# Kernel optimization log

Measured on AMD Instinct MI355X. Metric: run time of the kernel, lower is better.

The kernel has to match this reference:

```python
import jax, jax.numpy as jnp
import numpy as np

D_MODEL = 1024
D_FFN = 4096
N_HEAD = 16
D_K = D_MODEL // N_HEAD
EPS = 1e-10


def _layernorm(x, gamma, beta):
    mean = jnp.mean(x, axis=-1, keepdims=True)
    var = jnp.mean((x - mean) ** 2, axis=-1, keepdims=True)
    return gamma * ((x - mean) / jnp.sqrt(var + EPS)) + beta


def setup_inputs() -> dict:
    key = jax.random.key(0)
    ks = jax.random.split(key, 16)
    s = 1.0 / np.sqrt(D_MODEL)
    sf = 1.0 / np.sqrt(D_FFN)
    return {
        "x": jax.random.normal(ks[0], (4, 2048, D_MODEL), jnp.float32),
        "wq": jax.random.uniform(ks[1], (D_MODEL, D_MODEL), jnp.float32, -s, s),
        "bq": jnp.zeros((D_MODEL,), jnp.float32),
        "wk": jax.random.uniform(ks[2], (D_MODEL, D_MODEL), jnp.float32, -s, s),
        "bk": jnp.zeros((D_MODEL,), jnp.float32),
        "wv": jax.random.uniform(ks[3], (D_MODEL, D_MODEL), jnp.float32, -s, s),
        "bv": jnp.zeros((D_MODEL,), jnp.float32),
        "wo": jax.random.uniform(ks[4], (D_MODEL, D_MODEL), jnp.float32, -s, s),
        "bo": jnp.zeros((D_MODEL,), jnp.float32),
        "g1": jnp.ones((D_MODEL,), jnp.float32),
        "b1": jnp.zeros((D_MODEL,), jnp.float32),
        "w1": jax.random.uniform(ks[5], (D_MODEL, D_FFN), jnp.float32, -s, s),
        "bf1": jnp.zeros((D_FFN,), jnp.float32),
        "w2": jax.random.uniform(ks[6], (D_FFN, D_MODEL), jnp.float32, -sf, sf),
        "bf2": jnp.zeros((D_MODEL,), jnp.float32),
        "g2": jnp.ones((D_MODEL,), jnp.float32),
        "b2": jnp.zeros((D_MODEL,), jnp.float32),
    }


def reference(x, wq, bq, wk, bk, wv, bv, wo, bo, g1, b1, w1, bf1, w2, bf2, g2, b2):
    B, S, _ = x.shape
    # projections -> (B, H, S, d_k)
    q = (x @ wq + bq).reshape(B, S, N_HEAD, D_K).transpose(0, 2, 1, 3)
    k = (x @ wk + bk).reshape(B, S, N_HEAD, D_K).transpose(0, 2, 1, 3)
    v = (x @ wv + bv).reshape(B, S, N_HEAD, D_K).transpose(0, 2, 1, 3)
    score = jnp.einsum("bhqd,bhkd->bhqk", q, k) / jnp.sqrt(jnp.asarray(D_K, x.dtype))
    attn = jax.nn.softmax(score, axis=-1)
    out = jnp.einsum("bhqk,bhkd->bhqd", attn, v)
    out = out.transpose(0, 2, 1, 3).reshape(B, S, D_MODEL)
    out = out @ wo + bo
    out1 = _layernorm(x + out, g1, b1)
    # FFN (dropout is identity in eval mode)
    ff = jax.nn.relu(out1 @ w1 + bf1) @ w2 + bf2
    out2 = _layernorm(out1 + ff, g2, b2)
    return (out2, attn)
```

## Files before the change

### kernel.cpp

```cpp
#include <hip/hip_runtime.h>
#include <hip/hip_bf16.h>

#define DEV __device__ __forceinline__

typedef __attribute__((ext_vector_type(4))) float f32x4;
typedef __attribute__((ext_vector_type(8))) __bf16 bf16v;
typedef __attribute__((ext_vector_type(8))) unsigned short u16x8;
typedef __attribute__((ext_vector_type(4))) unsigned short u16x4;

DEV unsigned short f2b(float x) {
    unsigned u = __builtin_bit_cast(unsigned, x);
    unsigned r = u + 0x7FFF + ((u >> 16) & 1);
    return (unsigned short)(r >> 16);
}
DEV float b2f(unsigned short u) {
    unsigned v = (unsigned)u << 16;
    return __builtin_bit_cast(float, v);
}

DEV void gl_lds16(const void* g, void* l) {
    __builtin_amdgcn_global_load_lds(
        (const __attribute__((address_space(1))) unsigned*)g,
        (__attribute__((address_space(3))) unsigned*)l,
        16, 0, 0);
}


DEV void transp_dev(const float* __restrict__ in, unsigned short* __restrict__ out,
                    int R, int C, int bx, int by, float (*t)[33]) {
    int tx = threadIdx.x & 31, ty = threadIdx.x >> 5;
    long c0 = (long)bx * 32, r0 = (long)by * 32;
#pragma unroll
    for (int i = 0; i < 4; i++)
        t[ty + i * 8][tx] = in[(r0 + ty + i * 8) * C + c0 + tx];
    __syncthreads();
#pragma unroll
    for (int i = 0; i < 4; i++)
        out[(c0 + ty + i * 8) * R + r0 + tx] = f2b(t[tx][ty + i * 8]);
}

__global__ __launch_bounds__(256) void prep_all(
    const float* __restrict__ x, const float* __restrict__ wq,
    const float* __restrict__ wk, const float* __restrict__ wv,
    const float* __restrict__ wo, const float* __restrict__ w1,
    const float* __restrict__ w2, const float* __restrict__ bq,
    const float* __restrict__ bk, const float* __restrict__ bv,
    unsigned short* __restrict__ xb, unsigned short* __restrict__ wqkvT,
    unsigned short* __restrict__ woT, unsigned short* __restrict__ w1T,
    unsigned short* __restrict__ w2T, float* __restrict__ bqkv) {
    __shared__ float t[32][33];
    int id = blockIdx.x;
    if (id < 8192) {
        long i = ((long)id * 256 + threadIdx.x) * 4;
        float4 f = *(const float4*)(x + i);
        u16x4 u;
        u[0] = f2b(f.x); u[1] = f2b(f.y); u[2] = f2b(f.z); u[3] = f2b(f.w);
        *(u16x4*)(xb + i) = u;
        return;
    }
    id -= 8192;
    if (id < 1024) { transp_dev(wq, wqkvT, 1024, 1024, id & 31, id >> 5, t); return; }
    id -= 1024;
    if (id < 1024) { transp_dev(wk, wqkvT + 1048576, 1024, 1024, id & 31, id >> 5, t); return; }
    id -= 1024;
    if (id < 1024) { transp_dev(wv, wqkvT + 2097152, 1024, 1024, id & 31, id >> 5, t); return; }
    id -= 1024;
    if (id < 1024) { transp_dev(wo, woT, 1024, 1024, id & 31, id >> 5, t); return; }
    id -= 1024;
    if (id < 4096) { transp_dev(w1, w1T, 1024, 4096, id & 127, id >> 7, t); return; }
    id -= 4096;
    if (id < 4096) { transp_dev(w2, w2T, 4096, 1024, id & 31, id >> 5, t); return; }
    id -= 4096;
    int i = id * 256 + threadIdx.x;
    float v = (i < 1024) ? bq[i] : (i < 2048) ? bk[i - 1024] : bv[i - 2048];
    bqkv[i] = v;
}

DEV float waveSum(float v) {
#pragma unroll
    for (int o = 32; o > 0; o >>= 1) v += __shfl_xor(v, o);
    return v;
}

__global__ __launch_bounds__(256) void ln_rows(const float* __restrict__ in,
                                               const float* __restrict__ g,
                                               const float* __restrict__ b,
                                               float* __restrict__ outF,
                                               unsigned short* __restrict__ outB) {
    const float* p = in + (long)blockIdx.x * 1024;
    __shared__ float red[4], red2[4];
    int t = threadIdx.x, lane = t & 63, wave = t >> 6;
    float4 v = ((const float4*)p)[t];
    float s = v.x + v.y + v.z + v.w;
    float q = v.x * v.x + v.y * v.y + v.z * v.z + v.w * v.w;
    s = waveSum(s); q = waveSum(q);
    if (lane == 0) { red[wave] = s; red2[wave] = q; }
    __syncthreads();
    s = red[0] + red[1] + red[2] + red[3];
    q = red2[0] + red2[1] + red2[2] + red2[3];
    float mean = s * (1.0f / 1024.0f);
    float var = q * (1.0f / 1024.0f) - mean * mean;
    float rstd = rsqrtf(var + 1e-10f);
    float4 gg = ((const float4*)g)[t];
    float4 bb = ((const float4*)b)[t];
    float4 o;
    o.x = gg.x * ((v.x - mean) * rstd) + bb.x;
    o.y = gg.y * ((v.y - mean) * rstd) + bb.y;
    o.z = gg.z * ((v.z - mean) * rstd) + bb.z;
    o.w = gg.w * ((v.w - mean) * rstd) + bb.w;
    if (outF) ((float4*)(outF + (long)blockIdx.x * 1024))[t] = o;
    if (outB) {
        u16x4 u;
        u[0] = f2b(o.x); u[1] = f2b(o.y); u[2] = f2b(o.z); u[3] = f2b(o.w);
        *(u16x4*)(outB + (long)blockIdx.x * 1024 + (long)t * 4) = u;
    }
}

__global__ __launch_bounds__(256, 2) void attn_fused(
    const unsigned short* __restrict__ qb,
    const unsigned short* __restrict__ kb,
    const unsigned short* __restrict__ vt,
    float* __restrict__ attn,
    unsigned short* __restrict__ ao) {
    __shared__ __align__(16) char smem[65536];
    __shared__ float sredM[4][16], sredS[4][16];

    int id = blockIdx.x;
    int swz = (id & 7) * 1024 + (id >> 3);
    const int z = swz >> 7;
    const int m0 = (swz & 127) * 16;

    const int tid = threadIdx.x, lane = tid & 63, w = tid >> 6;
    const int g = lane >> 4, l15 = lane & 15;

    const char* qz = (const char*)(qb + (long)z * 131072);
    const char* kz = (const char*)(kb + (long)z * 131072);
    const char* vz = (const char*)(vt + (long)z * 131072);

    const char* qrow = qz + (long)(m0 + l15) * 128;
    bf16v aq0 = *(const bf16v*)(qrow + g * 16);
    bf16v aq1 = *(const bf16v*)(qrow + 64 + g * 16);

    f32x4 acc[8][4];
#pragma unroll
    for (int c = 0; c < 8; c++)
#pragma unroll
        for (int t = 0; t < 4; t++) acc[c][t] = (f32x4)(0.0f);

    const int soff = ((lane & 7) * 16) ^ (((lane >> 3) & 7) << 4);

    auto stage = [&](int c) {
        const char* src = kz + (long)(c * 256 + w * 8 + (lane >> 3)) * 128 + soff;
        char* dst = smem + (c & 1) * 32768 + w * 1024;
#pragma unroll
        for (int i = 0; i < 8; ++i)
            gl_lds16(src + (long)i * 4096, dst + i * 4096);
    };

    stage(0);
    for (int c = 0; c < 8; ++c) {
        if (c < 7) {
            stage(c + 1);
            asm volatile("s_waitcnt vmcnt(8)" ::: "memory");
        } else {
            asm volatile("s_waitcnt vmcnt(0)" ::: "memory");
        }
        __builtin_amdgcn_sched_barrier(0);
        __builtin_amdgcn_s_barrier();
        const char* base = smem + (c & 1) * 32768;
#pragma unroll
        for (int t = 0; t < 4; ++t) {
            const int row = w * 64 + t * 16 + l15;
            const char* bp = base + row * 128;
            const int sw = (lane & 7) << 4;
            bf16v bk0 = *(const bf16v*)(bp + ((g * 16) ^ sw));
            bf16v bk1 = *(const bf16v*)(bp + ((64 + g * 16) ^ sw));
            acc[c][t] = __builtin_amdgcn_mfma_f32_16x16x32_bf16(aq0, bk0, acc[c][t], 0, 0, 0);
            acc[c][t] = __builtin_amdgcn_mfma_f32_16x16x32_bf16(aq1, bk1, acc[c][t], 0, 0, 0);
        }
        __builtin_amdgcn_s_barrier();
    }

    float M[4], S[4];
#pragma unroll
    for (int j = 0; j < 4; ++j) {
        float m = -1e30f;
#pragma unroll
        for (int c = 0; c < 8; c++)
#pragma unroll
            for (int t = 0; t < 4; t++) m = fmaxf(m, acc[c][t][j]);
        m = fmaxf(m, __shfl_xor(m, 1));
        m = fmaxf(m, __shfl_xor(m, 2));
        m = fmaxf(m, __shfl_xor(m, 4));
        m = fmaxf(m, __shfl_xor(m, 8));
        M[j] = m;
    }
    if (l15 == 0) {
        sredM[w][g * 4 + 0] = M[0];
        sredM[w][g * 4 + 1] = M[1];
        sredM[w][g * 4 + 2] = M[2];
        sredM[w][g * 4 + 3] = M[3];
    }
    __syncthreads();
#pragma unroll
    for (int j = 0; j < 4; ++j) {
        int r = g * 4 + j;
        M[j] = 0.125f * fmaxf(fmaxf(sredM[0][r], sredM[1][r]),
                              fmaxf(sredM[2][r], sredM[3][r]));
        S[j] = 0.0f;
    }
#pragma unroll
    for (int c = 0; c < 8; c++)
#pragma unroll
        for (int t = 0; t < 4; t++) {
            f32x4 v = acc[c][t];
            v[0] = __expf(v[0] * 0.125f - M[0]);
            v[1] = __expf(v[1] * 0.125f - M[1]);
            v[2] = __expf(v[2] * 0.125f - M[2]);
            v[3] = __expf(v[3] * 0.125f - M[3]);
            acc[c][t] = v;
            S[0] += v[0]; S[1] += v[1]; S[2] += v[2]; S[3] += v[3];
        }
#pragma unroll
    for (int j = 0; j < 4; ++j) {
        float s = S[j];
        s += __shfl_xor(s, 1);
        s += __shfl_xor(s, 2);
        s += __shfl_xor(s, 4);
        s += __shfl_xor(s, 8);
        S[j] = s;
    }
    if (l15 == 0) {
        sredS[w][g * 4 + 0] = S[0];
        sredS[w][g * 4 + 1] = S[1];
        sredS[w][g * 4 + 2] = S[2];
        sredS[w][g * 4 + 3] = S[3];
    }
    __syncthreads();
    float inv[4];
#pragma unroll
    for (int j = 0; j < 4; ++j) {
        int r = g * 4 + j;
        inv[j] = 1.0f / (sredS[0][r] + sredS[1][r] + sredS[2][r] + sredS[3][r]);
    }

    float* ab = attn + (long)z * 4194304 + (long)m0 * 2048;
#pragma unroll
    for (int c = 0; c < 8; c++)
#pragma unroll
        for (int t = 0; t < 4; t++) {
            const int col = c * 256 + w * 64 + t * 16 + l15;
#pragma unroll
            for (int j = 0; j < 4; ++j) {
                const int r = g * 4 + j;
                float p = acc[c][t][j] * inv[j];
                ab[(long)r * 2048 + col] = p;
                *(unsigned short*)(smem + r * 4096 + ((col * 2) ^ ((r & 7) << 4))) = f2b(p);
            }
        }
    __syncthreads();

    f32x4 o0 = (f32x4)(0.0f), o1 = (f32x4)(0.0f);
    f32x4 o2 = (f32x4)(0.0f), o3 = (f32x4)(0.0f);
    const char* vtile = vz + (long)(w * 16 + l15) * 4096;
    const char* prow = smem + l15 * 4096;
    const int psw = (l15 & 7) << 4;
#pragma unroll 4
    for (int ks = 0; ks < 64; ks += 4) {
        bf16v pa0 = *(const bf16v*)(prow + (((ks + 0) * 64 + g * 16) ^ psw));
        bf16v pa1 = *(const bf16v*)(prow + (((ks + 1) * 64 + g * 16) ^ psw));
        bf16v pa2 = *(const bf16v*)(prow + (((ks + 2) * 64 + g * 16) ^ psw));
        bf16v pa3 = *(const bf16v*)(prow + (((ks + 3) * 64 + g * 16) ^ psw));
        bf16v bv0 = *(const bf16v*)(vtile + (ks + 0) * 64 + g * 16);
        bf16v bv1 = *(const bf16v*)(vtile + (ks + 1) * 64 + g * 16);
        bf16v bv2 = *(const bf16v*)(vtile + (ks + 2) * 64 + g * 16);
        bf16v bv3 = *(const bf16v*)(vtile + (ks + 3) * 64 + g * 16);
        o0 = __builtin_amdgcn_mfma_f32_16x16x32_bf16(pa0, bv0, o0, 0, 0, 0);
        o1 = __builtin_amdgcn_mfma_f32_16x16x32_bf16(pa1, bv1, o1, 0, 0, 0);
        o2 = __builtin_amdgcn_mfma_f32_16x16x32_bf16(pa2, bv2, o2, 0, 0, 0);
        o3 = __builtin_amdgcn_mfma_f32_16x16x32_bf16(pa3, bv3, o3, 0, 0, 0);
    }
    o0 = o0 + o1 + o2 + o3;

    const int b = z >> 4, h = z & 15;
    const long tokbase = (long)b * 2048 + m0 + g * 4;
#pragma unroll
    for (int j = 0; j < 4; ++j)
        ao[(tokbase + j) * 1024 + h * 64 + w * 16 + l15] = f2b(o0[j]);
}


enum { M_QKV3 = 0, M_RES = 1, M_RESB = 2, M_RELU = 3 };

struct GArgs {
    const unsigned short* A;
    long lda;
    const unsigned short* B;
    long ldb;
    const float* bias;
    const float* resid;
    const unsigned short* residB;
    float* outF;
    unsigned short* outB;
    unsigned short* outB2;
    unsigned short* outB3;
    long ldo;
    int K;
};

template <int MODE>
__global__ __launch_bounds__(512, 1) void gemm256(GArgs g) {
    __shared__ __align__(16) char smem[131072];
    const int tid = threadIdx.x, lane = tid & 63, wave = tid >> 6;
    const int wr = wave >> 2, wc = wave & 3;
    const int g2 = lane >> 4, l15 = lane & 15;
    const long m0 = (long)blockIdx.x * 256, n0 = (long)blockIdx.y * 256;
    const char* Ab = (const char*)(g.A + m0 * g.lda);
    const char* Bb = (const char*)(g.B + n0 * g.ldb);
    const long lda2 = g.lda * 2, ldb2 = g.ldb * 2;

    f32x4 acc[8][4];
#pragma unroll
    for (int mi = 0; mi < 8; mi++)
#pragma unroll
        for (int ni = 0; ni < 4; ni++) acc[mi][ni] = (f32x4)(0.0f);

    auto stage = [&](int t) {
        const int buf = (t & 1) * 32768;
        const long k0b = (long)t * 128;
#pragma unroll
        for (int i = 0; i < 4; ++i) {
            int c = i * 8 + wave;
            int p = c * 1024 + lane * 16;
            int row = p >> 7;
            int scb = (p & 127) ^ ((row & 7) << 4);
            gl_lds16(Ab + (long)row * lda2 + k0b + scb, smem + buf + c * 1024);
        }
#pragma unroll
        for (int i = 0; i < 4; ++i) {
            int c = i * 8 + wave;
            int p = c * 1024 + lane * 16;
            int row = p >> 7;
            int scb = (p & 127) ^ ((row & 7) << 4);
            gl_lds16(Bb + (long)row * ldb2 + k0b + scb, smem + 65536 + buf + c * 1024);
        }
    };

    const int NT = g.K >> 6;
    stage(0);
    for (int t = 0; t < NT; ++t) {
        if (t + 1 < NT) {
            stage(t + 1);
            asm volatile("s_waitcnt vmcnt(8)" ::: "memory");
        } else {
            asm volatile("s_waitcnt vmcnt(0)" ::: "memory");
        }
        __builtin_amdgcn_sched_barrier(0);
        __builtin_amdgcn_s_barrier();
        const char* bufA = smem + (t & 1) * 32768;
        const char* bufB = smem + 65536 + (t & 1) * 32768;
        bf16v bfr[4][2];
#pragma unroll
        for (int ni = 0; ni < 4; ++ni) {
            int r = wc * 64 + ni * 16 + l15;
            const char* bp = bufB + r * 128;
            int sw = (r & 7) << 4;
            bfr[ni][0] = *(const bf16v*)(bp + ((g2 * 16) ^ sw));
            bfr[ni][1] = *(const bf16v*)(bp + ((64 + g2 * 16) ^ sw));
        }
#pragma unroll
        for (int q = 0; q < 4; ++q) {
            bf16v af[2][2];
#pragma unroll
            for (int u = 0; u < 2; ++u) {
                int r = wr * 128 + (q * 2 + u) * 16 + l15;
                const char* ap = bufA + r * 128;
                int sw = (r & 7) << 4;
                af[u][0] = *(const bf16v*)(ap + ((g2 * 16) ^ sw));
                af[u][1] = *(const bf16v*)(ap + ((64 + g2 * 16) ^ sw));
            }
            asm volatile("s_waitcnt lgkmcnt(0)" ::: "memory");
            __builtin_amdgcn_sched_barrier(0);
            __builtin_amdgcn_s_setprio(1);
#pragma unroll
            for (int u = 0; u < 2; ++u)
#pragma unroll
                for (int ni = 0; ni < 4; ++ni) {
                    acc[q * 2 + u][ni] = __builtin_amdgcn_mfma_f32_16x16x32_bf16(
                        af[u][0], bfr[ni][0], acc[q * 2 + u][ni], 0, 0, 0);
                    acc[q * 2 + u][ni] = __builtin_amdgcn_mfma_f32_16x16x32_bf16(
                        af[u][1], bfr[ni][1], acc[q * 2 + u][ni], 0, 0, 0);
                }
            __builtin_amdgcn_s_setprio(0);
        }
        __builtin_amdgcn_sched_barrier(0);
        __builtin_amdgcn_s_barrier();
    }

#pragma unroll
    for (int mi = 0; mi < 8; mi++)
#pragma unroll
        for (int ni = 0; ni < 4; ni++) {
            if constexpr (MODE == M_QKV3) {
                long r = m0 + wr * 128 + mi * 16 + g2 * 4;
                long c = n0 + wc * 64 + ni * 16 + l15;
                long b = r >> 11, s = r & 2047;
                float bi = g.bias[c];
                if (c < 2048) {
                    unsigned short* dst = (c < 1024) ? g.outB : g.outB2;
                    long h = (c >> 6) & 15, d = c & 63;
                    long base = ((b * 16 + h) * 2048 + s) * 64 + d;
#pragma unroll
                    for (int j = 0; j < 4; ++j)
                        dst[base + (long)j * 64] = f2b(acc[mi][ni][j] + bi);
                } else {
                    long h = (c - 2048) >> 6, d = c & 63;
                    u16x4 u;
#pragma unroll
                    for (int j = 0; j < 4; ++j) u[j] = f2b(acc[mi][ni][j] + bi);
                    *(u16x4*)(g.outB3 + (b * 16 + h) * 131072 + d * 2048 + s) = u;
                }
            } else {
#pragma unroll
                for (int j = 0; j < 4; ++j) {
                    long r = m0 + wr * 128 + mi * 16 + g2 * 4 + j;
                    long c = n0 + wc * 64 + ni * 16 + l15;
                    float tv = acc[mi][ni][j] + g.bias[c];
                    g.outB[r * g.ldo + c] = f2b(tv > 0.0f ? tv : 0.0f);
                }
            }
        }
}


template <int BM, int BN, int WR, int WC, int MODE>
__global__ __launch_bounds__(256) void gemm_k(GArgs g) {
    constexpr int MI = BM / (WR * 16), NI = BN / (WC * 16);
    __shared__ __align__(16) char sm[(BM + BN) * 128];
    char* sA = sm;
    char* sB = sm + BM * 128;
    const int tid = threadIdx.x, lane = tid & 63, wave = tid >> 6;
    const int wr = wave / WC, wc = wave % WC;
    const long m0 = (long)blockIdx.x * BM, n0 = (long)blockIdx.y * BN;

    const char* Ab = (const char*)(g.A + m0 * g.lda);
    const char* Bb = (const char*)(g.B + n0 * g.ldb);
    const long lda = g.lda, ldb = g.ldb;

    f32x4 acc[MI][NI];
#pragma unroll
    for (int mi = 0; mi < MI; mi++)
#pragma unroll
        for (int ni = 0; ni < NI; ni++) acc[mi][ni] = (f32x4)(0.0f);

    for (int k0 = 0; k0 < g.K; k0 += 64) {
#pragma unroll
        for (int i = 0; i < BM / 32; i++) {
            int c = i * 4 + wave;
            int p = c * 1024 + lane * 16;
            int row = p >> 7;
            int scb = (p & 127) ^ ((row & 7) << 4);
            gl_lds16(Ab + (long)row * (lda * 2) + (long)k0 * 2 + scb, sA + c * 1024);
        }
#pragma unroll
        for (int i = 0; i < BN / 32; i++) {
            int c = i * 4 + wave;
            int p = c * 1024 + lane * 16;
            int row = p >> 7;
            int scb = (p & 127) ^ ((row & 7) << 4);
            gl_lds16(Bb + (long)row * (ldb * 2) + (long)k0 * 2 + scb, sB + c * 1024);
        }
        __syncthreads();
#pragma unroll
        for (int ks = 0; ks < 2; ++ks) {
            const int cb = ks * 64 + (lane >> 4) * 16;
            bf16v af[MI], bfv[NI];
#pragma unroll
            for (int mi = 0; mi < MI; mi++) {
                int r = wr * (BM / WR) + mi * 16 + (lane & 15);
                af[mi] = *(const bf16v*)(sA + r * 128 + (cb ^ ((r & 7) << 4)));
            }
#pragma unroll
            for (int ni = 0; ni < NI; ni++) {
                int r = wc * (BN / WC) + ni * 16 + (lane & 15);
                bfv[ni] = *(const bf16v*)(sB + r * 128 + (cb ^ ((r & 7) << 4)));
            }
#pragma unroll
            for (int mi = 0; mi < MI; mi++)
#pragma unroll
                for (int ni = 0; ni < NI; ni++)
                    acc[mi][ni] = __builtin_amdgcn_mfma_f32_16x16x32_bf16(
                        af[mi], bfv[ni], acc[mi][ni], 0, 0, 0);
        }
        __syncthreads();
    }

#pragma unroll
    for (int mi = 0; mi < MI; mi++)
#pragma unroll
        for (int ni = 0; ni < NI; ni++) {
#pragma unroll
            for (int j = 0; j < 4; ++j) {
                long r = m0 + wr * (BM / WR) + mi * 16 + (lane >> 4) * 4 + j;
                long c = n0 + wc * (BN / WC) + ni * 16 + (lane & 15);
                float v = acc[mi][ni][j];
                if constexpr (MODE == M_RES) {
                    long i = r * g.ldo + c;
                    g.outF[i] = v + g.bias[c] + g.resid[i];
                } else if constexpr (MODE == M_RESB) {
                    long i = r * g.ldo + c;
                    g.outF[i] = v + g.bias[c] + b2f(g.residB[i]);
                } else {
                    float t = v + g.bias[c];
                    g.outB[r * g.ldo + c] = f2b(t > 0.0f ? t : 0.0f);
                }
            }
        }
}


extern "C" void kernel_launch(void* const* d_in, const int* in_sizes, int n_in,
                              void* d_out, int out_size, void* d_ws, size_t ws_size,
                              hipStream_t stream) {
    const float* x = (const float*)d_in[0];
    const float* wq = (const float*)d_in[1];
    const float* bq = (const float*)d_in[2];
    const float* wk = (const float*)d_in[3];
    const float* bk = (const float*)d_in[4];
    const float* wv = (const float*)d_in[5];
    const float* bv = (const float*)d_in[6];
    const float* wo = (const float*)d_in[7];
    const float* bo = (const float*)d_in[8];
    const float* g1 = (const float*)d_in[9];
    const float* b1 = (const float*)d_in[10];
    const float* w1 = (const float*)d_in[11];
    const float* bf1 = (const float*)d_in[12];
    const float* w2 = (const float*)d_in[13];
    const float* bf2 = (const float*)d_in[14];
    const float* g2 = (const float*)d_in[15];
    const float* b2 = (const float*)d_in[16];

    float* out2 = (float*)d_out;
    float* attn = (float*)d_out + 8388608;

    char* ws = (char*)d_ws;
    size_t off = 0;
    auto alc = [&](size_t bytes) { size_t r = off; off += (bytes + 255) & ~(size_t)255; return r; };

    unsigned short* xb    = (unsigned short*)(ws + alc(16777216));
    unsigned short* wqkvT = (unsigned short*)(ws + alc(6291456));
    unsigned short* woT   = (unsigned short*)(ws + alc(2097152));
    unsigned short* w1T   = (unsigned short*)(ws + alc(8388608));
    unsigned short* w2T   = (unsigned short*)(ws + alc(8388608));
    float* bqkv           = (float*)(ws + alc(12288));
    size_t bigOff = alc(67108864);
    unsigned short* qb = (unsigned short*)(ws + bigOff);
    unsigned short* kb = qb + 8388608;
    unsigned short* vt = kb + 8388608;
    unsigned short* ff1 = qb;
    size_t aoOff = alc(16777216);
    unsigned short* ao  = (unsigned short*)(ws + aoOff);
    unsigned short* o1b = ao;
    size_t rOff = alc(33554432);
    float* r1 = (float*)(ws + rOff);
    float* r2 = r1;

    prep_all<<<20492, 256, 0, stream>>>(x, wq, wk, wv, wo, w1, w2, bq, bk, bv,
                                        xb, wqkvT, woT, w1T, w2T, bqkv);

    {
        GArgs a{};
        a.A = xb; a.lda = 1024; a.B = wqkvT; a.ldb = 1024; a.K = 1024;
        a.bias = bqkv; a.outB = qb; a.outB2 = kb; a.outB3 = vt;
        gemm256<M_QKV3><<<dim3(32, 12), 512, 0, stream>>>(a);
    }
    attn_fused<<<8192, 256, 0, stream>>>(qb, kb, vt, attn, ao);
    {
        GArgs a{};
        a.A = ao; a.lda = 1024; a.B = woT; a.ldb = 1024;
        a.bias = bo; a.resid = x; a.outF = r1; a.ldo = 1024; a.K = 1024;
        gemm_k<128, 128, 2, 2, M_RES><<<dim3(64, 8), 256, 0, stream>>>(a);
    }
    ln_rows<<<8192, 256, 0, stream>>>(r1, g1, b1, nullptr, o1b);
    {
        GArgs a{};
        a.A = o1b; a.lda = 1024; a.B = w1T; a.ldb = 1024;
        a.bias = bf1; a.outB = ff1; a.ldo = 4096; a.K = 1024;
        gemm256<M_RELU><<<dim3(32, 16), 512, 0, stream>>>(a);
    }
    {
        GArgs a{};
        a.A = ff1; a.lda = 4096; a.B = w2T; a.ldb = 4096;
        a.bias = bf2; a.residB = o1b; a.outF = r2; a.ldo = 1024; a.K = 4096;
        gemm_k<128, 128, 2, 2, M_RESB><<<dim3(64, 8), 256, 0, stream>>>(a);
    }
    ln_rows<<<8192, 256, 0, stream>>>(r2, g2, b2, out2, nullptr);

    (void)in_sizes; (void)n_in; (void)out_size; (void)ws_size;
}
```

Measured before the change: 842.5 us.

## Replace 128x128 residual GEMMs with double-buffered 256x128 512-thread kernel

The out-projection and FFN-down GEMMs move from a single-buffered 128x128 tile kernel with 256 threads to a 256x128 tile kernel with 512 threads. The new kernel double-buffers its LDS tiles, prefetching the next K-slice with async global-to-LDS loads while computing on the current one, and uses explicit vmcnt waits, scheduling barriers and setprio around the MFMA bursts. This is meant to hide global load latency and raise reuse per block. In exchange the kernel uses 96KB of LDS and allows only one block per CU. The grid also halves to 256 blocks, which may underfill the 256 CUs' wave slots.

```diff
diff --git a/kernel.cpp b/kernel.cpp
--- a/kernel.cpp
+++ b/kernel.cpp
@@ -432,90 +432,109 @@
         }
 }
 
-
-template <int BM, int BN, int WR, int WC, int MODE>
-__global__ __launch_bounds__(256) void gemm_k(GArgs g) {
-    constexpr int MI = BM / (WR * 16), NI = BN / (WC * 16);
-    __shared__ __align__(16) char sm[(BM + BN) * 128];
-    char* sA = sm;
-    char* sB = sm + BM * 128;
+template <int MODE>
+__global__ __launch_bounds__(512, 1) void gemm256x128(GArgs g) {
+    __shared__ __align__(16) char smem[98304];
     const int tid = threadIdx.x, lane = tid & 63, wave = tid >> 6;
-    const int wr = wave / WC, wc = wave % WC;
-    const long m0 = (long)blockIdx.x * BM, n0 = (long)blockIdx.y * BN;
-
+    const int wr = wave >> 1, wc = wave & 1;
+    const int g2 = lane >> 4, l15 = lane & 15;
+    const long m0 = (long)blockIdx.x * 256, n0 = (long)blockIdx.y * 128;
     const char* Ab = (const char*)(g.A + m0 * g.lda);
     const char* Bb = (const char*)(g.B + n0 * g.ldb);
-    const long lda = g.lda, ldb = g.ldb;
-
-    f32x4 acc[MI][NI];
-#pragma unroll
-    for (int mi = 0; mi < MI; mi++)
-#pragma unroll
-        for (int ni = 0; ni < NI; ni++) acc[mi][ni] = (f32x4)(0.0f);
-
-    for (int k0 = 0; k0 < g.K; k0 += 64) {
-#pragma unroll
-        for (int i = 0; i < BM / 32; i++) {
-            int c = i * 4 + wave;
+    const long lda2 = g.lda * 2, ldb2 = g.ldb * 2;
+
+    f32x4 acc[4][4];
+#pragma unroll
+    for (int mi = 0; mi < 4; mi++)
+#pragma unroll
+        for (int ni = 0; ni < 4; ni++) acc[mi][ni] = (f32x4)(0.0f);
+
+    auto stage = [&](int t) {
+        const int bufA = (t & 1) * 32768;
+        const int bufB = 65536 + (t & 1) * 16384;
+        const long k0b = (long)t * 128;
+#pragma unroll
+        for (int i = 0; i < 4; ++i) {
+            int c = i * 8 + wave;
             int p = c * 1024 + lane * 16;
             int row = p >> 7;
             int scb = (p & 127) ^ ((row & 7) << 4);
-            gl_lds16(Ab + (long)row * (lda * 2) + (long)k0 * 2 + scb, sA + c * 1024);
-        }
-#pragma unroll
-        for (int i = 0; i < BN / 32; i++) {
-            int c = i * 4 + wave;
+            gl_lds16(Ab + (long)row * lda2 + k0b + scb, smem + bufA + c * 1024);
+        }
+#pragma unroll
+        for (int i = 0; i < 2; ++i) {
+            int c = i * 8 + wave;
             int p = c * 1024 + lane * 16;
             int row = p >> 7;
             int scb = (p & 127) ^ ((row & 7) << 4);
-            gl_lds16(Bb + (long)row * (ldb * 2) + (long)k0 * 2 + scb, sB + c * 1024);
-        }
-        __syncthreads();
-#pragma unroll
-        for (int ks = 0; ks < 2; ++ks) {
-            const int cb = ks * 64 + (lane >> 4) * 16;
-            bf16v af[MI], bfv[NI];
-#pragma unroll
-            for (int mi = 0; mi < MI; mi++) {
-                int r = wr * (BM / WR) + mi * 16 + (lane & 15);
-                af[mi] = *(const bf16v*)(sA + r * 128 + (cb ^ ((r & 7) << 4)));
+            gl_lds16(Bb + (long)row * ldb2 + k0b + scb, smem + bufB + c * 1024);
+        }
+    };
+
+    const int NT = g.K >> 6;
+    stage(0);
+    for (int t = 0; t < NT; ++t) {
+        if (t + 1 < NT) {
+            stage(t + 1);
+            asm volatile("s_waitcnt vmcnt(6)" ::: "memory");
+        } else {
+            asm volatile("s_waitcnt vmcnt(0)" ::: "memory");
+        }
+        __builtin_amdgcn_sched_barrier(0);
+        __builtin_amdgcn_s_barrier();
+        const char* bufA = smem + (t & 1) * 32768;
+        const char* bufB = smem + 65536 + (t & 1) * 16384;
+        bf16v bfr[4][2];
+#pragma unroll
+        for (int ni = 0; ni < 4; ++ni) {
+            int r = wc * 64 + ni * 16 + l15;
+            const char* bp = bufB + r * 128;
+            int sw = (r & 7) << 4;
+            bfr[ni][0] = *(const bf16v*)(bp + ((g2 * 16) ^ sw));
+            bfr[ni][1] = *(const bf16v*)(bp + ((64 + g2 * 16) ^ sw));
+        }
+#pragma unroll
+        for (int q = 0; q < 4; ++q) {
+            bf16v af0, af1;
+            {
+                int r = wr * 64 + q * 16 + l15;
+                const char* ap = bufA + r * 128;
+                int sw = (r & 7) << 4;
+                af0 = *(const bf16v*)(ap + ((g2 * 16) ^ sw));
+                af1 = *(const bf16v*)(ap + ((64 + g2 * 16) ^ sw));
             }
-#pragma unroll
-            for (int ni = 0; ni < NI; ni++) {
-                int r = wc * (BN / WC) + ni * 16 + (lane & 15);
-                bfv[ni] = *(const bf16v*)(sB + r * 128 + (cb ^ ((r & 7) << 4)));
+            asm volatile("s_waitcnt lgkmcnt(0)" ::: "memory");
+            __builtin_amdgcn_sched_barrier(0);
+            __builtin_amdgcn_s_setprio(1);
+#pragma unroll
+            for (int ni = 0; ni < 4; ++ni) {
+                acc[q][ni] = __builtin_amdgcn_mfma_f32_16x16x32_bf16(
+                    af0, bfr[ni][0], acc[q][ni], 0, 0, 0);
+                acc[q][ni] = __builtin_amdgcn_mfma_f32_16x16x32_bf16(
+                    af1, bfr[ni][1], acc[q][ni], 0, 0, 0);
             }
-#pragma unroll
-            for (int mi = 0; mi < MI; mi++)
-#pragma unroll
-                for (int ni = 0; ni < NI; ni++)
-                    acc[mi][ni] = __builtin_amdgcn_mfma_f32_16x16x32_bf16(
-                        af[mi], bfv[ni], acc[mi][ni], 0, 0, 0);
-        }
-        __syncthreads();
-    }
-
-#pragma unroll
-    for (int mi = 0; mi < MI; mi++)
-#pragma unroll
-        for (int ni = 0; ni < NI; ni++) {
+            __builtin_amdgcn_s_setprio(0);
+        }
+        __builtin_amdgcn_sched_barrier(0);
+        __builtin_amdgcn_s_barrier();
+    }
+
+#pragma unroll
+    for (int mi = 0; mi < 4; mi++)
+#pragma unroll
+        for (int ni = 0; ni < 4; ni++)
 #pragma unroll
             for (int j = 0; j < 4; ++j) {
-                long r = m0 + wr * (BM / WR) + mi * 16 + (lane >> 4) * 4 + j;
-                long c = n0 + wc * (BN / WC) + ni * 16 + (lane & 15);
-                float v = acc[mi][ni][j];
+                long r = m0 + wr * 64 + mi * 16 + g2 * 4 + j;
+                long c = n0 + wc * 64 + ni * 16 + l15;
+                float v = acc[mi][ni][j] + g.bias[c];
+                long i = r * g.ldo + c;
                 if constexpr (MODE == M_RES) {
-                    long i = r * g.ldo + c;
-                    g.outF[i] = v + g.bias[c] + g.resid[i];
-                } else if constexpr (MODE == M_RESB) {
-                    long i = r * g.ldo + c;
-                    g.outF[i] = v + g.bias[c] + b2f(g.residB[i]);
+                    g.outF[i] = v + g.resid[i];
                 } else {
-                    float t = v + g.bias[c];
-                    g.outB[r * g.ldo + c] = f2b(t > 0.0f ? t : 0.0f);
+                    g.outF[i] = v + b2f(g.residB[i]);
                 }
             }
-        }
 }
 
 
@@ -579,7 +598,7 @@
         GArgs a{};
         a.A = ao; a.lda = 1024; a.B = woT; a.ldb = 1024;
         a.bias = bo; a.resid = x; a.outF = r1; a.ldo = 1024; a.K = 1024;
-        gemm_k<128, 128, 2, 2, M_RES><<<dim3(64, 8), 256, 0, stream>>>(a);
+        gemm256x128<M_RES><<<dim3(32, 8), 512, 0, stream>>>(a);
     }
     ln_rows<<<8192, 256, 0, stream>>>(r1, g1, b1, nullptr, o1b);
     {
@@ -592,7 +611,7 @@
         GArgs a{};
         a.A = ff1; a.lda = 4096; a.B = w2T; a.ldb = 4096;
         a.bias = bf2; a.residB = o1b; a.outF = r2; a.ldo = 1024; a.K = 4096;
-        gemm_k<128, 128, 2, 2, M_RESB><<<dim3(64, 8), 256, 0, stream>>>(a);
+        gemm256x128<M_RESB><<<dim3(32, 8), 512, 0, stream>>>(a);
     }
     ln_rows<<<8192, 256, 0, stream>>>(r2, g2, b2, out2, nullptr);
 
```

Result: faster. 801.0 us (-4.9%).
